# Optimization experiments

Measured on AMD Instinct MI355X. Metric: run time of the kernel, lower is better.

## Reference

```python
import jax, jax.numpy as jnp
import numpy as np

TEMPERATURE = 0.5


def setup_inputs() -> dict:
    key = jax.random.key(0)
    k1, k2 = jax.random.split(key)
    B, D = 8192, 128
    z_i = jax.random.normal(k1, (B, D), dtype=jnp.float32)
    z_j = jax.random.normal(k2, (B, D), dtype=jnp.float32)
    return {"z_i": z_i, "z_j": z_j}


def reference(z_i, z_j):
    B = z_i.shape[0]
    eps = 1e-12  # matches torch F.normalize default clamp
    zi = z_i / jnp.maximum(jnp.linalg.norm(z_i, axis=1, keepdims=True), eps)
    zj = z_j / jnp.maximum(jnp.linalg.norm(z_j, axis=1, keepdims=True), eps)
    reps = jnp.concatenate([zi, zj], axis=0)  # [2B, D], unit rows
    # cosine similarity of unit vectors == dot product -> single GEMM
    sim = reps @ reps.T  # [2B, 2B]
    n = 2 * B
    diag = jnp.eye(n, dtype=bool)
    sim = jnp.where(diag, -1e9, sim) / TEMPERATURE
    labels = jnp.concatenate([jnp.arange(B) + B, jnp.arange(B)])  # positive pair indices
    logp = jax.nn.log_softmax(sim, axis=1)
    loss = -jnp.mean(jnp.take_along_axis(logp, labels[:, None], axis=1))
    return loss
```

## Files before the change

### kernel.cpp

```cpp
#include <hip/hip_runtime.h>
#include <hip/hip_bf16.h>

#define NB 8192
#define ND 128
#define N2 16384

#define CPB 512
#define CTILE 64
#define NT (CPB / CTILE)
#define TILEB (CTILE * 128)

typedef __attribute__((ext_vector_type(4))) float f32x4;
typedef __attribute__((ext_vector_type(4))) int v4i;
typedef __attribute__((ext_vector_type(8))) int v8i;

static constexpr float SQRT_C_VAL = 1.69864368f;

__global__ __launch_bounds__(256) void nrm_kernel(const float* __restrict__ zi,
                                                  const float* __restrict__ zj,
                                                  unsigned short* __restrict__ reps8_u16,
                                                  float* __restrict__ pos,
                                                  float* __restrict__ ssum,
                                                  float* __restrict__ sdiag,
                                                  float* __restrict__ out) {
    const int gtid = blockIdx.x * 256 + threadIdx.x;
    if (gtid < N2) ssum[gtid] = 0.f;
    if (gtid == 0) out[0] = 0.f;
    const int pair = gtid >> 6;
    const int lane = threadIdx.x & 63;
    const float2 vi = *reinterpret_cast<const float2*>(zi + pair * ND + lane * 2);
    const float2 vj = *reinterpret_cast<const float2*>(zj + pair * ND + lane * 2);
    float ssi = vi.x * vi.x + vi.y * vi.y;
    float ssj = vj.x * vj.x + vj.y * vj.y;
#pragma unroll
    for (int m = 1; m < 64; m <<= 1) {
        ssi += __shfl_xor(ssi, m);
        ssj += __shfl_xor(ssj, m);
    }
    float ni = fmaxf(sqrtf(ssi), 1e-12f);
    float nj = fmaxf(sqrtf(ssj), 1e-12f);
    const float ii = 1.0f / ni, ij = 1.0f / nj;
    const float uix = vi.x * ii, uiy = vi.y * ii;
    const float ujx = vj.x * ij, ujy = vj.y * ij;
    float d = uix * ujx + uiy * ujy;
#pragma unroll
    for (int m = 1; m < 64; m <<= 1) d += __shfl_xor(d, m);
    if (lane == 0) pos[pair] = d;
    const int pki = __builtin_amdgcn_cvt_pk_fp8_f32(uix * SQRT_C_VAL, uiy * SQRT_C_VAL, 0, false);
    const int pkj = __builtin_amdgcn_cvt_pk_fp8_f32(ujx * SQRT_C_VAL, ujy * SQRT_C_VAL, 0, false);
    reps8_u16[pair * 64 + lane] = (unsigned short)(pki & 0xFFFF);
    reps8_u16[(NB + pair) * 64 + lane] = (unsigned short)(pkj & 0xFFFF);
    const float fi0 = __builtin_amdgcn_cvt_f32_fp8(pki, 0);
    const float fi1 = __builtin_amdgcn_cvt_f32_fp8(pki, 1);
    const float fj0 = __builtin_amdgcn_cvt_f32_fp8(pkj, 0);
    const float fj1 = __builtin_amdgcn_cvt_f32_fp8(pkj, 1);
    float sqi = fi0 * fi0 + fi1 * fi1;
    float sqj = fj0 * fj0 + fj1 * fj1;
#pragma unroll
    for (int m = 1; m < 64; m <<= 1) {
        sqi += __shfl_xor(sqi, m);
        sqj += __shfl_xor(sqj, m);
    }
    if (lane == 0) {
        sdiag[pair] = sqi;
        sdiag[NB + pair] = sqj;
    }
}

__device__ inline void gload_lds16(const void* g, void* l) {
    __builtin_amdgcn_global_load_lds(
        (const __attribute__((address_space(1))) void*)g,
        (__attribute__((address_space(3))) void*)l, 16, 0, 0);
}

__global__ __launch_bounds__(512, 4) void sim_kernel(const char* __restrict__ reps8,
                                                     float* __restrict__ ssum) {
    __shared__ __align__(16) char lds[4][TILEB];
    const int tid = threadIdx.x;
    const int lane = tid & 63;
    const int wid = tid >> 6;
    const int l15 = lane & 15;
    const int l4 = lane >> 4;
    const int rb = blockIdx.x * 256;
    const int cb = blockIdx.y * CPB;
    const int qb = rb + wid * 32;

    v8i qf[2];
#pragma unroll
    for (int g = 0; g < 2; ++g)
        qf[g] = *reinterpret_cast<const v8i*>(
            reps8 + (size_t)(qb + g * 16 + l15) * 128 + l4 * 32);
    __builtin_amdgcn_sched_barrier(0);
    asm volatile("s_waitcnt vmcnt(0)" ::: "memory");
    __builtin_amdgcn_sched_barrier(0);

    f32x4 sacc[2];
#pragma unroll
    for (int g = 0; g < 2; ++g) sacc[g] = {0.f, 0.f, 0.f, 0.f};

    const int m_s = tid >> 4;
    const int sp_s = tid & 15;
    const int s_s = sp_s ^ ((m_s & 3) << 1);
    const char* srcq = reps8 + (size_t)(cb + 2 * m_s + (s_s & 1)) * 128 + (s_s >> 1) * 16;

    auto stage = [&](int t) {
        char* dst = &lds[t & 3][wid * 1024];
        gload_lds16(srcq + (size_t)t * TILEB, dst);
    };

    const int h = l15 >> 1;
    const int sloA = (4 * l4 + (l15 & 1)) ^ ((h & 3) << 1);
    const int rdlo = h * 256 + sloA * 16;
    const int rdhi = h * 256 + (sloA ^ 2) * 16;

    stage(0);
    stage(1);
    stage(2);

#pragma unroll 1
    for (int t = 0; t < NT; ++t) {
        if (t <= NT - 3) {
            asm volatile("s_waitcnt vmcnt(2)" ::: "memory");
        } else if (t == NT - 2) {
            asm volatile("s_waitcnt vmcnt(1)" ::: "memory");
        } else {
            asm volatile("s_waitcnt vmcnt(0)" ::: "memory");
        }
        __builtin_amdgcn_s_barrier();
        if (t + 3 < NT) stage(t + 3);

        const char* lbase = lds[t & 3];
#pragma unroll
        for (int cc = 0; cc < 4; ++cc) {
            const int cg = (cc + wid) & 3;
            const v4i lo = *reinterpret_cast<const v4i*>(lbase + rdlo + cg * 2048);
            const v4i hi = *reinterpret_cast<const v4i*>(lbase + rdhi + cg * 2048);
            const v8i kf = __builtin_shufflevector(lo, hi, 0, 1, 2, 3, 4, 5, 6, 7);
            const f32x4 z4 = {0.f, 0.f, 0.f, 0.f};
            __builtin_amdgcn_s_setprio(1);
            f32x4 acc0 = __builtin_amdgcn_mfma_scale_f32_16x16x128_f8f6f4(
                qf[0], kf, z4, 0, 0, 0, 0x7F7F7F7F, 0, 0x7F7F7F7F);
            f32x4 acc1 = __builtin_amdgcn_mfma_scale_f32_16x16x128_f8f6f4(
                qf[1], kf, z4, 0, 0, 0, 0x7F7F7F7F, 0, 0x7F7F7F7F);
            __builtin_amdgcn_s_setprio(0);
            f32x4 e0, e1;
#pragma unroll
            for (int r = 0; r < 4; ++r) {
                e0[r] = __builtin_amdgcn_exp2f(acc0[r]);
                e1[r] = __builtin_amdgcn_exp2f(acc1[r]);
            }
            sacc[0] += e0;
            sacc[1] += e1;
        }
    }

#pragma unroll
    for (int g = 0; g < 2; ++g) {
#pragma unroll
        for (int r = 0; r < 4; ++r) {
#pragma unroll
            for (int m = 1; m < 16; m <<= 1) sacc[g][r] += __shfl_xor(sacc[g][r], m);
        }
    }
    if (l15 == 0) {
#pragma unroll
        for (int g = 0; g < 2; ++g)
#pragma unroll
            for (int r = 0; r < 4; ++r)
                atomicAdd(&ssum[qb + g * 16 + l4 * 4 + r], sacc[g][r]);
    }
}

__global__ __launch_bounds__(1024) void fin_kernel(const float* __restrict__ ssum,
                                                   const float* __restrict__ pos,
                                                   const float* __restrict__ sdiag,
                                                   float* __restrict__ out) {
    const int tid = threadIdx.x;
    const int r0 = blockIdx.x * (N2 / 16);
    float acc = 0.f;
    for (int i = tid; i < N2 / 16; i += 1024) {
        const int r = r0 + i;
        const int p = (r < NB) ? r : r - NB;
        acc += logf(ssum[r] - exp2f(sdiag[r])) - 2.0f * pos[p];
    }
#pragma unroll
    for (int m = 1; m < 64; m <<= 1) acc += __shfl_xor(acc, m);
    __shared__ float red[16];
    const int wid = tid >> 6, lane = tid & 63;
    if (lane == 0) red[wid] = acc;
    __syncthreads();
    if (wid == 0) {
        float v = (lane < 16) ? red[lane] : 0.f;
#pragma unroll
        for (int m = 1; m < 16; m <<= 1) v += __shfl_xor(v, m);
        if (lane == 0) atomicAdd(out, v / (float)N2);
    }
}

extern "C" void kernel_launch(void* const* d_in, const int* in_sizes, int n_in,
                              void* d_out, int out_size, void* d_ws, size_t ws_size,
                              hipStream_t stream) {
    const float* zi = (const float*)d_in[0];
    const float* zj = (const float*)d_in[1];
    float* out = (float*)d_out;
    char* ws = (char*)d_ws;

    char* reps8 = ws;
    float* pos = (float*)(ws + (size_t)N2 * ND);
    float* ssum = pos + NB;
    float* sdiag = ssum + N2;

    nrm_kernel<<<NB / 4, 256, 0, stream>>>(zi, zj, (unsigned short*)reps8, pos, ssum, sdiag, out);
    dim3 grid(N2 / 256, N2 / CPB);
    sim_kernel<<<grid, 512, 0, stream>>>(reps8, ssum);
    fin_kernel<<<16, 1024, 0, stream>>>(ssum, pos, sdiag, out);
}
```

Baseline: 53.43 us.

## Switch similarity tile to 32x32x64 FP8 scaled MFMA with K-split accumulation

Replaces the pair of 16x16x128 scaled FP8 MFMAs per 16-column group with two chained 32x32x64 MFMAs per 32-column group. The K dimension is split into two halves that accumulate into one 16-register accumulator. LDS fragment addressing, the query fragment loads and the final cross-lane reduction and atomics are reworked for the 32x32 output layout. The occupancy hint drops from 4 to 2 blocks per CU to make room for the larger accumulators. The aim is fewer MFMA issues and LDS reads per output element, at the cost of more registers and a dependent MFMA chain before the exp2.

```diff
diff --git a/kernel.cpp b/kernel.cpp
--- a/kernel.cpp
+++ b/kernel.cpp
@@ -11,6 +11,7 @@
 #define TILEB (CTILE * 128)
 
 typedef __attribute__((ext_vector_type(4))) float f32x4;
+typedef __attribute__((ext_vector_type(16))) float f32x16;
 typedef __attribute__((ext_vector_type(4))) int v4i;
 typedef __attribute__((ext_vector_type(8))) int v8i;
 
@@ -73,30 +74,27 @@
         (__attribute__((address_space(3))) void*)l, 16, 0, 0);
 }
 
-__global__ __launch_bounds__(512, 4) void sim_kernel(const char* __restrict__ reps8,
+__global__ __launch_bounds__(512, 2) void sim_kernel(const char* __restrict__ reps8,
                                                      float* __restrict__ ssum) {
     __shared__ __align__(16) char lds[4][TILEB];
     const int tid = threadIdx.x;
     const int lane = tid & 63;
     const int wid = tid >> 6;
-    const int l15 = lane & 15;
-    const int l4 = lane >> 4;
+    const int l31 = lane & 31;
+    const int h5 = lane >> 5;
     const int rb = blockIdx.x * 256;
     const int cb = blockIdx.y * CPB;
     const int qb = rb + wid * 32;
 
-    v8i qf[2];
-#pragma unroll
-    for (int g = 0; g < 2; ++g)
-        qf[g] = *reinterpret_cast<const v8i*>(
-            reps8 + (size_t)(qb + g * 16 + l15) * 128 + l4 * 32);
+    v8i qfA = *reinterpret_cast<const v8i*>(reps8 + (size_t)(qb + l31) * 128 + h5 * 32);
+    v8i qfB = *reinterpret_cast<const v8i*>(reps8 + (size_t)(qb + l31) * 128 + 64 + h5 * 32);
     __builtin_amdgcn_sched_barrier(0);
     asm volatile("s_waitcnt vmcnt(0)" ::: "memory");
     __builtin_amdgcn_sched_barrier(0);
 
-    f32x4 sacc[2];
-#pragma unroll
-    for (int g = 0; g < 2; ++g) sacc[g] = {0.f, 0.f, 0.f, 0.f};
+    f32x16 sacc;
+#pragma unroll
+    for (int r = 0; r < 16; ++r) sacc[r] = 0.f;
 
     const int m_s = tid >> 4;
     const int sp_s = tid & 15;
@@ -108,10 +106,10 @@
         gload_lds16(srcq + (size_t)t * TILEB, dst);
     };
 
-    const int h = l15 >> 1;
-    const int sloA = (4 * l4 + (l15 & 1)) ^ ((h & 3) << 1);
-    const int rdlo = h * 256 + sloA * 16;
-    const int rdhi = h * 256 + (sloA ^ 2) * 16;
+    const int w = l31 >> 1;
+    const int sA = (4 * h5 + (l31 & 1)) ^ ((w & 3) << 1);
+    const int rdLo = w * 256 + sA * 16;
+    const int rdHi = w * 256 + (sA ^ 2) * 16;
 
     stage(0);
     stage(1);
@@ -131,43 +129,40 @@
 
         const char* lbase = lds[t & 3];
 #pragma unroll
-        for (int cc = 0; cc < 4; ++cc) {
-            const int cg = (cc + wid) & 3;
-            const v4i lo = *reinterpret_cast<const v4i*>(lbase + rdlo + cg * 2048);
-            const v4i hi = *reinterpret_cast<const v4i*>(lbase + rdhi + cg * 2048);
-            const v8i kf = __builtin_shufflevector(lo, hi, 0, 1, 2, 3, 4, 5, 6, 7);
-            const f32x4 z4 = {0.f, 0.f, 0.f, 0.f};
+        for (int cc = 0; cc < 2; ++cc) {
+            const int cg = (cc + wid) & 1;
+            const char* cgb = lbase + cg * 4096;
+            const v4i a0 = *reinterpret_cast<const v4i*>(cgb + rdLo);
+            const v4i a1 = *reinterpret_cast<const v4i*>(cgb + rdHi);
+            const v4i b0 = *reinterpret_cast<const v4i*>(cgb + rdLo + 128);
+            const v4i b1 = *reinterpret_cast<const v4i*>(cgb + rdHi + 128);
+            const v8i kfA = __builtin_shufflevector(a0, a1, 0, 1, 2, 3, 4, 5, 6, 7);
+            const v8i kfB = __builtin_shufflevector(b0, b1, 0, 1, 2, 3, 4, 5, 6, 7);
+            f32x16 acc;
+#pragma unroll
+            for (int r = 0; r < 16; ++r) acc[r] = 0.f;
             __builtin_amdgcn_s_setprio(1);
-            f32x4 acc0 = __builtin_amdgcn_mfma_scale_f32_16x16x128_f8f6f4(
-                qf[0], kf, z4, 0, 0, 0, 0x7F7F7F7F, 0, 0x7F7F7F7F);
-            f32x4 acc1 = __builtin_amdgcn_mfma_scale_f32_16x16x128_f8f6f4(
-                qf[1], kf, z4, 0, 0, 0, 0x7F7F7F7F, 0, 0x7F7F7F7F);
+            acc = __builtin_amdgcn_mfma_scale_f32_32x32x64_f8f6f4(
+                qfA, kfA, acc, 0, 0, 0, 0x7F7F7F7F, 0, 0x7F7F7F7F);
+            acc = __builtin_amdgcn_mfma_scale_f32_32x32x64_f8f6f4(
+                qfB, kfB, acc, 0, 0, 0, 0x7F7F7F7F, 0, 0x7F7F7F7F);
             __builtin_amdgcn_s_setprio(0);
-            f32x4 e0, e1;
-#pragma unroll
-            for (int r = 0; r < 4; ++r) {
-                e0[r] = __builtin_amdgcn_exp2f(acc0[r]);
-                e1[r] = __builtin_amdgcn_exp2f(acc1[r]);
-            }
-            sacc[0] += e0;
-            sacc[1] += e1;
+            f32x16 e;
+#pragma unroll
+            for (int r = 0; r < 16; ++r) e[r] = __builtin_amdgcn_exp2f(acc[r]);
+            sacc += e;
         }
     }
 
 #pragma unroll
-    for (int g = 0; g < 2; ++g) {
-#pragma unroll
-        for (int r = 0; r < 4; ++r) {
-#pragma unroll
-            for (int m = 1; m < 16; m <<= 1) sacc[g][r] += __shfl_xor(sacc[g][r], m);
-        }
-    }
-    if (l15 == 0) {
-#pragma unroll
-        for (int g = 0; g < 2; ++g)
-#pragma unroll
-            for (int r = 0; r < 4; ++r)
-                atomicAdd(&ssum[qb + g * 16 + l4 * 4 + r], sacc[g][r]);
+    for (int r = 0; r < 16; ++r) {
+#pragma unroll
+        for (int m = 1; m < 32; m <<= 1) sacc[r] += __shfl_xor(sacc[r], m);
+    }
+    if (l31 == 0) {
+#pragma unroll
+        for (int r = 0; r < 16; ++r)
+            atomicAdd(&ssum[qb + (r & 3) + 8 * (r >> 2) + 4 * h5], sacc[r]);
     }
 }
 
```

Measured after the change: 59.99 us. 12.3% more time.
